# Kernel optimization log

Measured on AMD Instinct MI355X. Metric: run time of the kernel, lower is better.

## Reference

```python
import jax, jax.numpy as jnp
import numpy as np

N, P, E, D, T, R, K = 4096, 32768, 4096, 128, 3, 4, 16
CURRENT_TIME = 1.0


def setup_inputs() -> dict:
    key = jax.random.key(0)
    ks = jax.random.split(key, 12)
    pairs = jax.random.randint(ks[0], (P, 2), 0, N)
    adj = (jax.random.randint(ks[1], (N, N), 0, 100) == 0).astype(jnp.int32)
    adj = jnp.maximum(adj, adj.T) * (1 - jnp.eye(N, dtype=jnp.int32))
    neigh_idx = jax.random.randint(ks[2], (N, R, K), 0, N)
    node_type = jax.random.randint(ks[3], (N,), 0, T)
    # event timestamps far in the past so the decay sum stays O(1)
    t_events = -(jax.random.uniform(ks[4], (E,), dtype=jnp.float32) * 100.0 + 50.0)
    node_embeds = 0.1 * jax.random.normal(ks[5], (N, D), dtype=jnp.float32)
    W_proj = 0.1 * jax.random.normal(ks[6], (T, D, D), dtype=jnp.float32)
    W_beta = 0.1 * jax.random.normal(ks[7], (R, D, D), dtype=jnp.float32)
    b_beta = 0.1 * jax.random.normal(ks[8], (R, D), dtype=jnp.float32)
    decay_theta = jnp.float32(0.1)
    q1 = jnp.float32(0.5)
    q2 = jnp.float32(0.1)
    return dict(pairs=pairs, adj=adj, neigh_idx=neigh_idx, node_type=node_type,
                t_events=t_events, node_embeds=node_embeds, W_proj=W_proj,
                W_beta=W_beta, b_beta=b_beta, decay_theta=decay_theta, q1=q1, q2=q2)


def _forward(pairs, adj, neigh_idx, node_type, t_events, node_embeds,
             W_proj, W_beta, b_beta, decay_theta, q1, q2):
    n_nodes, d = node_embeds.shape
    adj_f = adj.astype(node_embeds.dtype)
    pm, pn = pairs[:, 0], pairs[:, 1]

    # --- HistoricalEdgeModule: type-specific projection + global decay sum ---
    proj_all = jnp.einsum('nd,tde->tne', node_embeds, W_proj)      # [T,N,D]
    proj = proj_all[node_type, jnp.arange(n_nodes)]                # [N,D]
    diff = proj[pm] - proj[pn]
    gamma_base = -jnp.sqrt(jnp.sum(diff * diff, axis=-1))          # [P]
    sum_alpha = jnp.sum(jnp.exp(-decay_theta * (CURRENT_TIME - t_events)))
    lambda_hist = gamma_base + sum_alpha                           # [P]

    # --- TriadicClosureModule: clustering coeff + common-neighbor sum ---
    deg = adj_f.sum(axis=1)
    tri = jnp.sum((adj_f @ adj_f) * adj_f.T, axis=1)               # diag(A^3)
    denom = deg * (deg - 1.0)
    denom = jnp.where(denom == 0, 1e-6, denom)
    C = 2.0 * tri / denom                                          # [N]
    common = adj_f[pm] * adj_f[pn]                                 # [P,N] common-neighbor mask
    Csum = common @ C                                              # [P]
    g = -jnp.sum((node_embeds[pm] - node_embeds[pn]) ** 2, axis=-1)
    lambda_tri = Csum * g                                          # [P]

    # --- NeighborInfluenceModule: per-relation mean agg -> macro sigmoid ---
    h_r = node_embeds[neigh_idx].mean(axis=2)                      # [N,R,D]
    h_agg = jnp.einsum('nrd,rde->nre', h_r, W_beta) + b_beta       # [N,R,D]
    eps = jax.nn.sigmoid(h_agg.mean(axis=1))                       # [N,D]
    lambda_neigh = jnp.sum(eps[pm] * eps[pn], axis=-1) / d         # [P]

    lam = jnp.exp(lambda_hist + lambda_tri + lambda_neigh)
    return jax.nn.sigmoid(q1 * lam + q2)


def reference(pairs, adj, neigh_idx, node_type, t_events, node_embeds,
              W_proj, W_beta, b_beta, decay_theta, q1, q2):
    return _forward(pairs, adj, neigh_idx, node_type, t_events, node_embeds,
                    W_proj, W_beta, b_beta, decay_theta, q1, q2)
```

## Files before the change

### kernel.cpp

```cpp
#include <hip/hip_runtime.h>
#include <math.h>

#define N_NODES 4096
#define DIM     128
#define NPAIRS  32768
#define NEVENTS 4096
#define NTYPES  3
#define NREL    4
#define NNEIGH  16
#define WORDS   64
#define MAXDEG  192


#define PA_MASK_END  (N_NODES / 4)
#define PA_PROJ_END  (PA_MASK_END + N_NODES)
#define PA_HR_END    (PA_PROJ_END + N_NODES * NREL * DIM / (256 * 4))
#define PA_TOTAL     (PA_HR_END + 1)

__global__ __launch_bounds__(256) void k_phaseA(const int* __restrict__ adj,
                                                unsigned long long* __restrict__ mask,
                                                float* __restrict__ degf,
                                                unsigned short* __restrict__ nbr,
                                                const float* __restrict__ x,
                                                const int* __restrict__ ntype,
                                                const float* __restrict__ Wp,
                                                float* __restrict__ proj,
                                                const int* __restrict__ nidx,
                                                float* __restrict__ h,
                                                const float* __restrict__ t_events,
                                                const float* __restrict__ theta_p,
                                                float* __restrict__ salpha) {
    __shared__ float smem[1280];
    int b = blockIdx.x;

    if (b < PA_MASK_END) {
        int wave = threadIdx.x >> 6;
        int lane = threadIdx.x & 63;
        int row  = b * 4 + wave;
        const int4* arow = (const int4*)(adj + (size_t)row * N_NODES);
        unsigned long long myw = 0ULL;
        #pragma unroll
        for (int ch = 0; ch < 16; ++ch) {
            int4 v = arow[ch * 64 + lane];
            unsigned long long b0 = __ballot(v.x != 0);
            unsigned long long b1 = __ballot(v.y != 0);
            unsigned long long b2 = __ballot(v.z != 0);
            unsigned long long b3 = __ballot(v.w != 0);
            if ((lane >> 2) == ch) {
                int c = lane & 3;
                myw = (c == 0) ? b0 : (c == 1) ? b1 : (c == 2) ? b2 : b3;
            }
        }
        mask[(size_t)row * WORDS + lane] = myw;
        int pc = (int)__popcll(myw);
        int scan = pc;
        #pragma unroll
        for (int off = 1; off < 64; off <<= 1) {
            int nv = __shfl_up(scan, off);
            if (lane >= off) scan += nv;
        }
        int excl = scan - pc;
        if (lane == 63) degf[row] = (float)scan;
        unsigned short* nl = nbr + (size_t)row * MAXDEG;
        int jb = (lane >> 2) * 256 + (lane & 3);
        unsigned long long ww = myw;
        int o = excl;
        while (ww) {
            int bit = __ffsll(ww) - 1;
            nl[o++] = (unsigned short)(jb + bit * 4);
            ww &= ww - 1;
        }

    } else if (b < PA_PROJ_END) {
        int n = b - PA_MASK_END;
        int eg = threadIdx.x & 31;
        int kg = threadIdx.x >> 5;
        float* xs = smem;
        float* part = smem + 128;
        if (threadIdx.x < 32)
            ((float4*)xs)[threadIdx.x] = ((const float4*)(x + (size_t)n * DIM))[threadIdx.x];
        __syncthreads();
        int t = ntype[n];
        const float4* W4 = (const float4*)(Wp + (size_t)t * DIM * DIM) + eg;
        float4 acc = {0.f, 0.f, 0.f, 0.f};
        int k0 = kg * 16;
        #pragma unroll
        for (int kk = 0; kk < 16; ++kk) {
            float xk = xs[k0 + kk];
            float4 w = W4[(size_t)(k0 + kk) * 32];
            acc.x += xk * w.x; acc.y += xk * w.y; acc.z += xk * w.z; acc.w += xk * w.w;
        }
        ((float4*)(part + kg * 128))[eg] = acc;
        __syncthreads();
        if (threadIdx.x < 128) {
            int e = threadIdx.x;
            float s = part[e] + part[128 + e] + part[256 + e] + part[384 + e]
                    + part[512 + e] + part[640 + e] + part[768 + e] + part[896 + e];
            proj[(size_t)n * DIM + e] = s;
        }

    } else if (b < PA_HR_END) {
        int tid = (b - PA_PROJ_END) * 256 + threadIdx.x;
        int dq = tid & 31;
        int nr = tid >> 5;
        const int4* idx4 = (const int4*)(nidx + (size_t)nr * NNEIGH);
        int4 i0 = idx4[0], i1 = idx4[1], i2 = idx4[2], i3 = idx4[3];
        const float4* xb = (const float4*)x;
        float4 s = {0.f, 0.f, 0.f, 0.f};
        float4 v;
        #define ACC4(i) v = xb[(size_t)(i) * 32 + dq]; s.x += v.x; s.y += v.y; s.z += v.z; s.w += v.w;
        ACC4(i0.x) ACC4(i0.y) ACC4(i0.z) ACC4(i0.w)
        ACC4(i1.x) ACC4(i1.y) ACC4(i1.z) ACC4(i1.w)
        ACC4(i2.x) ACC4(i2.y) ACC4(i2.z) ACC4(i2.w)
        ACC4(i3.x) ACC4(i3.y) ACC4(i3.z) ACC4(i3.w)
        #undef ACC4
        float4 r;
        r.x = s.x * (1.0f / 16.0f); r.y = s.y * (1.0f / 16.0f);
        r.z = s.z * (1.0f / 16.0f); r.w = s.w * (1.0f / 16.0f);
        ((float4*)h)[(size_t)nr * 32 + dq] = r;

    } else {
        float th = theta_p[0];
        float acc = 0.f;
        for (int i = threadIdx.x; i < NEVENTS; i += 256)
            acc += expf(-th * (1.0f - t_events[i]));
        smem[threadIdx.x] = acc;
        __syncthreads();
        for (int s = 128; s > 0; s >>= 1) {
            if (threadIdx.x < s) smem[threadIdx.x] += smem[threadIdx.x + s];
            __syncthreads();
        }
        if (threadIdx.x == 0) salpha[0] = smem[0];
    }
}

__global__ __launch_bounds__(256) void k_clust(const unsigned long long* __restrict__ mask,
                                               const float* __restrict__ degf,
                                               const unsigned short* __restrict__ nbr,
                                               float* __restrict__ C) {
    __shared__ unsigned int wacc[4];
    int node = blockIdx.x;
    int wave = threadIdx.x >> 6;
    int lane = threadIdx.x & 63;
    unsigned long long my = mask[(size_t)node * WORDS + lane];
    int dg = (int)degf[node];
    const unsigned short* nlist = nbr + (size_t)node * MAXDEG;
    int pidx = wave + 4 * lane;
    int pre = (lane < 48) ? (int)nlist[pidx] : 0;
    int nit = (dg - wave + 3) >> 2;
    if (nit < 0) nit = 0;
    unsigned int acc = 0;
    #pragma unroll 4
    for (int t = 0; t < nit; ++t) {
        int j = __shfl(pre, t);
        acc += __popcll(my & mask[(size_t)j * WORDS + lane]);
    }
    for (int off = 32; off > 0; off >>= 1) acc += __shfl_xor(acc, off);
    if (lane == 0) wacc[wave] = acc;
    __syncthreads();
    if (threadIdx.x == 0) {
        float tri = (float)(wacc[0] + wacc[1] + wacc[2] + wacc[3]);
        float dgF = (float)dg;
        float denom = dgF * (dgF - 1.0f);
        if (denom == 0.0f) denom = 1e-6f;
        C[node] = 2.0f * tri / denom;
    }
}

__global__ __launch_bounds__(256) void k_eps(const float* __restrict__ h,
                                             const float* __restrict__ Wb,
                                             const float* __restrict__ bb,
                                             float* __restrict__ eps) {
    __shared__ float hs[4 * 512];
    __shared__ float part[8 * 4 * 128];
    int base = blockIdx.x * 4;
    int eg = threadIdx.x & 31;
    int g  = threadIdx.x >> 5;
    int e0 = eg * 4;

    const float4* hsrc = (const float4*)(h + (size_t)base * NREL * DIM);
    float4* hs4 = (float4*)hs;
    hs4[threadIdx.x]       = hsrc[threadIdx.x];
    hs4[threadIdx.x + 256] = hsrc[threadIdx.x + 256];
    __syncthreads();

    const float* W = Wb + (size_t)(g * 64) * DIM + e0;
    float4 a0 = {0,0,0,0}, a1 = {0,0,0,0}, a2 = {0,0,0,0}, a3 = {0,0,0,0};
    int hq = g * 16;
    #pragma unroll 2
    for (int kk = 0; kk < 16; ++kk) {
        float4 h0 = hs4[0 * 128 + hq + kk];
        float4 h1 = hs4[1 * 128 + hq + kk];
        float4 h2 = hs4[2 * 128 + hq + kk];
        float4 h3 = hs4[3 * 128 + hq + kk];
        float4 w0 = *(const float4*)&W[(size_t)(kk * 4 + 0) * DIM];
        float4 w1 = *(const float4*)&W[(size_t)(kk * 4 + 1) * DIM];
        float4 w2 = *(const float4*)&W[(size_t)(kk * 4 + 2) * DIM];
        float4 w3 = *(const float4*)&W[(size_t)(kk * 4 + 3) * DIM];
        a0.x += h0.x*w0.x + h0.y*w1.x + h0.z*w2.x + h0.w*w3.x;
        a0.y += h0.x*w0.y + h0.y*w1.y + h0.z*w2.y + h0.w*w3.y;
        a0.z += h0.x*w0.z + h0.y*w1.z + h0.z*w2.z + h0.w*w3.z;
        a0.w += h0.x*w0.w + h0.y*w1.w + h0.z*w2.w + h0.w*w3.w;
        a1.x += h1.x*w0.x + h1.y*w1.x + h1.z*w2.x + h1.w*w3.x;
        a1.y += h1.x*w0.y + h1.y*w1.y + h1.z*w2.y + h1.w*w3.y;
        a1.z += h1.x*w0.z + h1.y*w1.z + h1.z*w2.z + h1.w*w3.z;
        a1.w += h1.x*w0.w + h1.y*w1.w + h1.z*w2.w + h1.w*w3.w;
        a2.x += h2.x*w0.x + h2.y*w1.x + h2.z*w2.x + h2.w*w3.x;
        a2.y += h2.x*w0.y + h2.y*w1.y + h2.z*w2.y + h2.w*w3.y;
        a2.z += h2.x*w0.z + h2.y*w1.z + h2.z*w2.z + h2.w*w3.z;
        a2.w += h2.x*w0.w + h2.y*w1.w + h2.z*w2.w + h2.w*w3.w;
        a3.x += h3.x*w0.x + h3.y*w1.x + h3.z*w2.x + h3.w*w3.x;
        a3.y += h3.x*w0.y + h3.y*w1.y + h3.z*w2.y + h3.w*w3.y;
        a3.z += h3.x*w0.z + h3.y*w1.z + h3.z*w2.z + h3.w*w3.z;
        a3.w += h3.x*w0.w + h3.y*w1.w + h3.z*w2.w + h3.w*w3.w;
    }
    float4* p4 = (float4*)part;
    p4[(g * 4 + 0) * 32 + eg] = a0;
    p4[(g * 4 + 1) * 32 + eg] = a1;
    p4[(g * 4 + 2) * 32 + eg] = a2;
    p4[(g * 4 + 3) * 32 + eg] = a3;
    __syncthreads();
    #pragma unroll
    for (int rep = 0; rep < 2; ++rep) {
        int idx = threadIdx.x + rep * 256;
        int m = idx >> 7;
        int e = idx & 127;
        float s = 0.f;
        #pragma unroll
        for (int gg = 0; gg < 8; ++gg)
            s += part[(gg * 4 + m) * 128 + e];
        float bsum = bb[e] + bb[DIM + e] + bb[2 * DIM + e] + bb[3 * DIM + e];
        float v = (s + bsum) * 0.25f;
        eps[(size_t)(base + m) * DIM + e] = 1.0f / (1.0f + expf(-v));
    }
}

__global__ __launch_bounds__(256) void k_pairs(const int* __restrict__ pairs,
                                               const unsigned long long* __restrict__ mask,
                                               const float* __restrict__ C,
                                               const float* __restrict__ proj,
                                               const float* __restrict__ eps,
                                               const float* __restrict__ x,
                                               const float* __restrict__ salpha_p,
                                               const float* __restrict__ q1p,
                                               const float* __restrict__ q2p,
                                               float* __restrict__ out) {
    int wave = threadIdx.x >> 6;
    int lane = threadIdx.x & 63;
    int p = blockIdx.x * 4 + wave;
    int pm = pairs[p * 2];
    int pn = pairs[p * 2 + 1];

    unsigned long long cw = mask[(size_t)pm * WORDS + lane] & mask[(size_t)pn * WORDS + lane];
    float csum = 0.f;
    int jbase = (lane >> 2) * 256 + (lane & 3);
    while (cw) {
        int bit = __ffsll(cw) - 1;
        csum += C[jbase + bit * 4];
        cw &= cw - 1;
    }

    const float2* Am = (const float2*)(proj + (size_t)pm * DIM);
    const float2* An = (const float2*)(proj + (size_t)pn * DIM);
    const float2* Xm = (const float2*)(x    + (size_t)pm * DIM);
    const float2* Xn = (const float2*)(x    + (size_t)pn * DIM);
    const float2* Em = (const float2*)(eps  + (size_t)pm * DIM);
    const float2* En = (const float2*)(eps  + (size_t)pn * DIM);
    float2 am = Am[lane], an = An[lane];
    float2 xm = Xm[lane], xn = Xn[lane];
    float2 em = Em[lane], en = En[lane];

    float dpx = am.x - an.x, dpy = am.y - an.y;
    float s1 = dpx * dpx + dpy * dpy;
    float dxx = xm.x - xn.x, dxy = xm.y - xn.y;
    float s2 = dxx * dxx + dxy * dxy;
    float s3 = em.x * en.x + em.y * en.y;

    for (int off = 32; off > 0; off >>= 1) {
        s1 += __shfl_xor(s1, off);
        s2 += __shfl_xor(s2, off);
        s3 += __shfl_xor(s3, off);
        csum += __shfl_xor(csum, off);
    }
    if (lane == 0) {
        float lhist  = -sqrtf(s1) + salpha_p[0];
        float ltri   = csum * (-s2);
        float lneigh = s3 * (1.0f / 128.0f);
        float lam = expf(lhist + ltri + lneigh);
        float z = q1p[0] * lam + q2p[0];
        out[p] = 1.0f / (1.0f + expf(-z));
    }
}

extern "C" void kernel_launch(void* const* d_in, const int* in_sizes, int n_in,
                              void* d_out, int out_size, void* d_ws, size_t ws_size,
                              hipStream_t stream) {
    const int*   pairs    = (const int*)d_in[0];
    const int*   adj      = (const int*)d_in[1];
    const int*   nidx     = (const int*)d_in[2];
    const int*   ntype    = (const int*)d_in[3];
    const float* t_events = (const float*)d_in[4];
    const float* x        = (const float*)d_in[5];
    const float* Wp       = (const float*)d_in[6];
    const float* Wb       = (const float*)d_in[7];
    const float* bb       = (const float*)d_in[8];
    const float* theta    = (const float*)d_in[9];
    const float* q1       = (const float*)d_in[10];
    const float* q2       = (const float*)d_in[11];
    float* out = (float*)d_out;

    char* ws = (char*)d_ws;
    unsigned long long* mask = (unsigned long long*)(ws + 0);
    float* deg    = (float*)(ws + 2097152);
    float* C      = (float*)(ws + 2113536);
    float* proj   = (float*)(ws + 2129920);
    float* eps    = (float*)(ws + 4227072);
    float* salpha = (float*)(ws + 6324224);
    float* h      = (float*)(ws + 6324352);
    unsigned short* nbr = (unsigned short*)(ws + 14712960);

    hipLaunchKernelGGL(k_phaseA, dim3(PA_TOTAL),    dim3(256), 0, stream,
                       adj, mask, deg, nbr, x, ntype, Wp, proj, nidx, h, t_events, theta, salpha);
    hipLaunchKernelGGL(k_clust,  dim3(N_NODES),     dim3(256), 0, stream, mask, deg, nbr, C);
    hipLaunchKernelGGL(k_eps,    dim3(N_NODES / 4), dim3(256), 0, stream, h, Wb, bb, eps);
    hipLaunchKernelGGL(k_pairs,  dim3(NPAIRS / 4),  dim3(256), 0, stream,
                       pairs, mask, C, proj, eps, x, salpha, q1, q2, out);
}
```

Before: 77.39 us.

## Split adjacency bitmask packing across more blocks and build neighbor lists in clustering kernel

The bitmask build now gives each adjacency row to four blocks, one 256-int4 chunk per wave, with nontemporal loads, instead of one wave looping over 16 chunks of a row. The degree and neighbor-list construction moves out of phase A into k_clust, which rebuilds the list in shared memory from the mask row it already loads, and the global deg and nbr buffers go away. The aim is more memory-level parallelism on the 64 MB adjacency read and less global write traffic. The cost is four times as many phase-A blocks and a serial scan plus list build per clustering block, with a __syncthreads that stalls three of the four waves.

```diff
diff --git a/kernel.cpp b/kernel.cpp
--- a/kernel.cpp
+++ b/kernel.cpp
@@ -12,15 +12,15 @@
 #define MAXDEG  192
 
 
-#define PA_MASK_END  (N_NODES / 4)
+typedef int nt_int4 __attribute__((ext_vector_type(4)));
+
+#define PA_MASK_END  (N_NODES * 4)
 #define PA_PROJ_END  (PA_MASK_END + N_NODES)
 #define PA_HR_END    (PA_PROJ_END + N_NODES * NREL * DIM / (256 * 4))
 #define PA_TOTAL     (PA_HR_END + 1)
 
 __global__ __launch_bounds__(256) void k_phaseA(const int* __restrict__ adj,
                                                 unsigned long long* __restrict__ mask,
-                                                float* __restrict__ degf,
-                                                unsigned short* __restrict__ nbr,
                                                 const float* __restrict__ x,
                                                 const int* __restrict__ ntype,
                                                 const float* __restrict__ Wp,
@@ -30,45 +30,23 @@
                                                 const float* __restrict__ t_events,
                                                 const float* __restrict__ theta_p,
                                                 float* __restrict__ salpha) {
-    __shared__ float smem[1280];
+    __shared__ __align__(16) float smem[1280];
     int b = blockIdx.x;
 
     if (b < PA_MASK_END) {
+        int row = b >> 2;
+        int q   = b & 3;
         int wave = threadIdx.x >> 6;
         int lane = threadIdx.x & 63;
-        int row  = b * 4 + wave;
-        const int4* arow = (const int4*)(adj + (size_t)row * N_NODES);
-        unsigned long long myw = 0ULL;
-        #pragma unroll
-        for (int ch = 0; ch < 16; ++ch) {
-            int4 v = arow[ch * 64 + lane];
-            unsigned long long b0 = __ballot(v.x != 0);
-            unsigned long long b1 = __ballot(v.y != 0);
-            unsigned long long b2 = __ballot(v.z != 0);
-            unsigned long long b3 = __ballot(v.w != 0);
-            if ((lane >> 2) == ch) {
-                int c = lane & 3;
-                myw = (c == 0) ? b0 : (c == 1) ? b1 : (c == 2) ? b2 : b3;
-            }
-        }
-        mask[(size_t)row * WORDS + lane] = myw;
-        int pc = (int)__popcll(myw);
-        int scan = pc;
-        #pragma unroll
-        for (int off = 1; off < 64; off <<= 1) {
-            int nv = __shfl_up(scan, off);
-            if (lane >= off) scan += nv;
-        }
-        int excl = scan - pc;
-        if (lane == 63) degf[row] = (float)scan;
-        unsigned short* nl = nbr + (size_t)row * MAXDEG;
-        int jb = (lane >> 2) * 256 + (lane & 3);
-        unsigned long long ww = myw;
-        int o = excl;
-        while (ww) {
-            int bit = __ffsll(ww) - 1;
-            nl[o++] = (unsigned short)(jb + bit * 4);
-            ww &= ww - 1;
+        const nt_int4* arow = (const nt_int4*)(adj + (size_t)row * N_NODES);
+        nt_int4 v = __builtin_nontemporal_load(&arow[q * 256 + wave * 64 + lane]);
+        unsigned long long b0 = __ballot(v.x != 0);
+        unsigned long long b1 = __ballot(v.y != 0);
+        unsigned long long b2 = __ballot(v.z != 0);
+        unsigned long long b3 = __ballot(v.w != 0);
+        if (lane < 4) {
+            unsigned long long w = (lane == 0) ? b0 : (lane == 1) ? b1 : (lane == 2) ? b2 : b3;
+            mask[(size_t)row * WORDS + (q * 4 + wave) * 4 + lane] = w;
         }
 
     } else if (b < PA_PROJ_END) {
@@ -135,18 +113,39 @@
 }
 
 __global__ __launch_bounds__(256) void k_clust(const unsigned long long* __restrict__ mask,
-                                               const float* __restrict__ degf,
-                                               const unsigned short* __restrict__ nbr,
                                                float* __restrict__ C) {
+    __shared__ unsigned short nl[MAXDEG];
     __shared__ unsigned int wacc[4];
+    __shared__ int sdeg;
     int node = blockIdx.x;
     int wave = threadIdx.x >> 6;
     int lane = threadIdx.x & 63;
     unsigned long long my = mask[(size_t)node * WORDS + lane];
-    int dg = (int)degf[node];
-    const unsigned short* nlist = nbr + (size_t)node * MAXDEG;
+
+    if (wave == 0) {
+        int pc = (int)__popcll(my);
+        int scan = pc;
+        #pragma unroll
+        for (int off = 1; off < 64; off <<= 1) {
+            int nv = __shfl_up(scan, off);
+            if (lane >= off) scan += nv;
+        }
+        int excl = scan - pc;
+        if (lane == 63) sdeg = scan;
+        int jb = (lane >> 2) * 256 + (lane & 3);
+        unsigned long long ww = my;
+        int o = excl;
+        while (ww) {
+            int bit = __ffsll(ww) - 1;
+            if (o < MAXDEG) nl[o] = (unsigned short)(jb + bit * 4);
+            ++o;
+            ww &= ww - 1;
+        }
+    }
+    __syncthreads();
+    int dg = sdeg;
     int pidx = wave + 4 * lane;
-    int pre = (lane < 48) ? (int)nlist[pidx] : 0;
+    int pre = (lane < 48) ? (int)nl[pidx] : 0;
     int nit = (dg - wave + 3) >> 2;
     if (nit < 0) nit = 0;
     unsigned int acc = 0;
@@ -311,17 +310,15 @@
 
     char* ws = (char*)d_ws;
     unsigned long long* mask = (unsigned long long*)(ws + 0);
-    float* deg    = (float*)(ws + 2097152);
     float* C      = (float*)(ws + 2113536);
     float* proj   = (float*)(ws + 2129920);
     float* eps    = (float*)(ws + 4227072);
     float* salpha = (float*)(ws + 6324224);
     float* h      = (float*)(ws + 6324352);
-    unsigned short* nbr = (unsigned short*)(ws + 14712960);
 
     hipLaunchKernelGGL(k_phaseA, dim3(PA_TOTAL),    dim3(256), 0, stream,
-                       adj, mask, deg, nbr, x, ntype, Wp, proj, nidx, h, t_events, theta, salpha);
-    hipLaunchKernelGGL(k_clust,  dim3(N_NODES),     dim3(256), 0, stream, mask, deg, nbr, C);
+                       adj, mask, x, ntype, Wp, proj, nidx, h, t_events, theta, salpha);
+    hipLaunchKernelGGL(k_clust,  dim3(N_NODES),     dim3(256), 0, stream, mask, C);
     hipLaunchKernelGGL(k_eps,    dim3(N_NODES / 4), dim3(256), 0, stream, h, Wb, bb, eps);
     hipLaunchKernelGGL(k_pairs,  dim3(NPAIRS / 4),  dim3(256), 0, stream,
                        pairs, mask, C, proj, eps, x, salpha, q1, q2, out);
```

Result: slower. 83.50 us (median of 2 runs) (+7.9%).
